# Kernel tuning notes

Hardware: AMD Instinct MI355X
Metric: run time of the kernel (lower is better)

The kernel has to match this reference:

```python
import jax, jax.numpy as jnp
import numpy as np

B, L, C, D = 32, 256, 16, 128
WORD_VOCAB, CHR_VOCAB = 50000, 128


def conv1d(x, w, b):
    # x: [N, D, T], w: [D_out, D_in, 3], torch Conv1d (cross-correlation), padding=1
    y = jax.lax.conv_general_dilated(x, w, window_strides=(1,), padding=[(1, 1)],
                                     dimension_numbers=('NCH', 'OIH', 'NCH'))
    return y + b[None, :, None]


def setup_inputs() -> dict:
    key = jax.random.key(0)
    k1, k2, k3, k4, k5, k6, k7, k8 = jax.random.split(key, 8)
    word_vector = jax.random.randint(k1, (B, L), 0, WORD_VOCAB)
    words_in_char = jax.random.randint(k2, (B, L, C), 0, CHR_VOCAB)
    # embedding tables, padding_idx=0 -> row 0 is zeros
    word_table = (jax.random.normal(k3, (WORD_VOCAB, D), jnp.float32) * 0.02).at[0].set(0.0)
    chr_table = (jax.random.normal(k4, (CHR_VOCAB, D), jnp.float32) * 0.02).at[0].set(0.0)
    scale = 1.0 / np.sqrt(D * 3)
    conv_chr_w = jax.random.normal(k5, (D, D, 3), jnp.float32) * scale
    conv_chr_b = jax.random.normal(k6, (D,), jnp.float32) * scale
    conv_word_w = jax.random.normal(k7, (D, D, 3), jnp.float32) * scale
    conv_word_b = jax.random.normal(k8, (D,), jnp.float32) * scale
    return dict(word_vector=word_vector, words_in_char=words_in_char,
                word_table=word_table, chr_table=chr_table,
                conv_chr_w=conv_chr_w, conv_chr_b=conv_chr_b,
                conv_word_w=conv_word_w, conv_word_b=conv_word_b)


def reference(word_vector, words_in_char, word_table, chr_table,
              conv_chr_w, conv_chr_b, conv_word_w, conv_word_b):
    # --- char path (batched version of the per-word Python loop) ---
    chr_emb = chr_table[words_in_char]                       # [B, L, C, D]
    x = chr_emb.reshape(B * L, C, D).transpose(0, 2, 1)      # [B*L, D, C]
    word_conv = conv1d(x, conv_chr_w, conv_chr_b)            # [B*L, D, C]
    char_feats = word_conv.max(axis=2).reshape(B, L, D)      # max over char positions
    # --- word path ---
    word_emb = word_table[word_vector]                       # [B, L, D]
    out = conv1d(word_emb.transpose(0, 2, 1), conv_word_w, conv_word_b)  # [B, D, L]
    # stack both branch outputs into one array: [2, B, D, L]
    return jnp.stack([out, char_feats.transpose(0, 2, 1)])
```

## Files before the change

### kernel.cpp

```cpp
#include <hip/hip_runtime.h>
#include <hip/hip_bf16.h>

typedef __attribute__((ext_vector_type(8))) short short8;
typedef __attribute__((ext_vector_type(4))) float float4_t;

#define NB 32
#define NL 256
#define NC 16
#define ND 128
#define OUT_PLANE (NB * ND * NL)

__device__ inline unsigned short f2bf(float f) {
    union { float f; unsigned int i; } c;
    c.f = f;
    unsigned int r = c.i + 0x7FFFu + ((c.i >> 16) & 1u);
    return (unsigned short)(r >> 16);
}

__global__ void make_frags(const float* __restrict__ Wc,
                           const float* __restrict__ Ww,
                           unsigned short* __restrict__ out) {
    int i = blockIdx.x * 256 + threadIdx.x;
    const int half = 12 * 8 * 64 * 8;
    const float* W = (i < half) ? Wc : Ww;
    int ii = (i < half) ? i : i - half;
    int j    = ii & 7;
    int lane = (ii >> 3) & 63;
    int nt   = (ii >> 9) & 7;
    int s    = ii >> 12;
    int dout = nt * 16 + (lane & 15);
    int t    = s >> 2;
    int k    = (s & 3) * 32 + ((lane >> 4) & 3) * 8 + j;
    out[i] = f2bf(W[(dout * 128 + k) * 3 + t]);
}

__global__ __launch_bounds__(128, 2) void char_kernel(
    const int* __restrict__ wic, const float* __restrict__ chrT,
    const unsigned short* __restrict__ frags,
    const float* __restrict__ bias,
    float* __restrict__ out1) {
    __shared__ unsigned short X[18 * 136];
    const int tid  = threadIdx.x;
    const int wave = tid >> 6, lane = tid & 63;
    const int m = lane & 15, quad = lane >> 4;

    for (int p = tid; p < 136; p += 128) { X[p] = 0; X[17 * 136 + p] = 0; }

    short8 bfrag[12][4];
#pragma unroll
    for (int s = 0; s < 12; ++s)
#pragma unroll
        for (int p = 0; p < 4; ++p) {
            int nt = wave * 4 + p;
            bfrag[s][p] =
                *(const short8*)(frags + (((s * 8 + nt) * 64 + lane) << 3));
        }
    float bb[4];
#pragma unroll
    for (int p = 0; p < 4; ++p) bb[p] = bias[wave * 64 + p * 16 + m];

    const int r = tid >> 3, seg = tid & 7;
    for (int wl = 0; wl < 8; ++wl) {
        int w = blockIdx.x * 8 + wl;
        __syncthreads();
        int idx = wic[w * 16 + r];
        const float4_t* src = (const float4_t*)(chrT + idx * 128 + seg * 16);
        unsigned short tmp[16];
#pragma unroll
        for (int q = 0; q < 4; ++q) {
            float4_t f = src[q];
            tmp[q * 4 + 0] = f2bf(f.x);
            tmp[q * 4 + 1] = f2bf(f.y);
            tmp[q * 4 + 2] = f2bf(f.z);
            tmp[q * 4 + 3] = f2bf(f.w);
        }
        *(short8*)&X[(r + 1) * 136 + seg * 16]     = *(const short8*)&tmp[0];
        *(short8*)&X[(r + 1) * 136 + seg * 16 + 8] = *(const short8*)&tmp[8];
        __syncthreads();

        float4_t acc[4];
#pragma unroll
        for (int p = 0; p < 4; ++p) acc[p] = (float4_t){0.f, 0.f, 0.f, 0.f};
#pragma unroll
        for (int s = 0; s < 12; ++s) {
            int row = m + (s >> 2);
            short8 a =
                *(const short8*)&X[row * 136 + (s & 3) * 32 + quad * 8];
#pragma unroll
            for (int p = 0; p < 4; ++p)
                acc[p] = __builtin_amdgcn_mfma_f32_16x16x32_bf16(
                    a, bfrag[s][p], acc[p], 0, 0, 0);
        }

        int b = w >> 8, l = w & 255;
        float* obase = out1 + b * (ND * NL) + l;
#pragma unroll
        for (int p = 0; p < 4; ++p) {
            float v = fmaxf(fmaxf(acc[p].x, acc[p].y),
                            fmaxf(acc[p].z, acc[p].w));
            v = fmaxf(v, __shfl_xor(v, 16, 64));
            v = fmaxf(v, __shfl_xor(v, 32, 64));
            v += bb[p];
            if (quad == 0) obase[(wave * 64 + p * 16 + m) * NL] = v;
        }
    }
}

__global__ __launch_bounds__(128, 2) void word_kernel(
    const int* __restrict__ wv, const float* __restrict__ wordT,
    const unsigned short* __restrict__ frags,
    const float* __restrict__ bias,
    float* __restrict__ out0) {
    __shared__ unsigned short X[18 * 136];
    const int tid  = threadIdx.x;
    const int wave = tid >> 6, lane = tid & 63;
    const int m = lane & 15, quad = lane >> 4;

    short8 bfrag[12][4];
#pragma unroll
    for (int s = 0; s < 12; ++s)
#pragma unroll
        for (int p = 0; p < 4; ++p) {
            int nt = wave * 4 + p;
            bfrag[s][p] = *(const short8*)(frags + 49152 +
                                           (((s * 8 + nt) * 64 + lane) << 3));
        }
    float bb[4];
#pragma unroll
    for (int p = 0; p < 4; ++p) bb[p] = bias[wave * 64 + p * 16 + m];

    for (int tl = 0; tl < 2; ++tl) {
        int tile = blockIdx.x * 2 + tl;
        int b = tile >> 4, l0 = (tile & 15) << 4;
        __syncthreads();
        for (int i = tid; i < 144; i += 128) {
            int rr = i >> 3, sg = i & 7;
            int l = l0 + rr - 1;
            int idx = (l >= 0 && l < NL) ? wv[b * NL + l] : 0;
            const float4_t* src = (const float4_t*)(wordT + idx * 128 + sg * 16);
            unsigned short tmp[16];
#pragma unroll
            for (int q = 0; q < 4; ++q) {
                float4_t f = src[q];
                tmp[q * 4 + 0] = f2bf(f.x);
                tmp[q * 4 + 1] = f2bf(f.y);
                tmp[q * 4 + 2] = f2bf(f.z);
                tmp[q * 4 + 3] = f2bf(f.w);
            }
            *(short8*)&X[rr * 136 + sg * 16]     = *(const short8*)&tmp[0];
            *(short8*)&X[rr * 136 + sg * 16 + 8] = *(const short8*)&tmp[8];
        }
        __syncthreads();

        float4_t acc[4];
#pragma unroll
        for (int p = 0; p < 4; ++p) acc[p] = (float4_t){0.f, 0.f, 0.f, 0.f};
#pragma unroll
        for (int s = 0; s < 12; ++s) {
            short8 a = *(const short8*)&X[(m + (s >> 2)) * 136 +
                                          (s & 3) * 32 + quad * 8];
#pragma unroll
            for (int p = 0; p < 4; ++p)
                acc[p] = __builtin_amdgcn_mfma_f32_16x16x32_bf16(
                    a, bfrag[s][p], acc[p], 0, 0, 0);
        }

        float* obase = out0 + b * (ND * NL) + l0 + quad * 4;
#pragma unroll
        for (int p = 0; p < 4; ++p) {
            int dout = wave * 64 + p * 16 + m;
            float4_t pk;
            pk.x = acc[p].x + bb[p];
            pk.y = acc[p].y + bb[p];
            pk.z = acc[p].z + bb[p];
            pk.w = acc[p].w + bb[p];
            *(float4_t*)&obase[dout * NL] = pk;
        }
    }
}

extern "C" void kernel_launch(void* const* d_in, const int* in_sizes, int n_in,
                              void* d_out, int out_size, void* d_ws,
                              size_t ws_size, hipStream_t stream) {
    const int* word_vector   = (const int*)d_in[0];
    const int* words_in_char = (const int*)d_in[1];
    const float* word_table  = (const float*)d_in[2];
    const float* chr_table   = (const float*)d_in[3];
    const float* conv_chr_w  = (const float*)d_in[4];
    const float* conv_chr_b  = (const float*)d_in[5];
    const float* conv_word_w = (const float*)d_in[6];
    const float* conv_word_b = (const float*)d_in[7];
    float* out            = (float*)d_out;
    unsigned short* frags = (unsigned short*)d_ws;

    make_frags<<<384, 256, 0, stream>>>(conv_chr_w, conv_word_w, frags);
    char_kernel<<<1024, 128, 0, stream>>>(words_in_char, chr_table, frags,
                                          conv_chr_b, out + OUT_PLANE);
    word_kernel<<<256, 128, 0, stream>>>(word_vector, word_table, frags,
                                         conv_word_b, out);
}
```

Before: 110.1 us.

## Merge char and word conv kernels and double-buffer char embedding gathers

Combines the char and word convolution kernels into one launch, using block-index ranges to pick the branch, so both branches run concurrently and one launch is removed. The char branch now double-buffers shared memory: it prefetches the next word's embedding rows and indices into registers while the MFMA work runs on the current buffer. The word branch gives each block one tile instead of two, which doubles the number of word blocks and repeats the weight-fragment loads per tile. The cost is twice the shared memory per block and more live registers, which could reduce occupancy.

```diff
diff --git a/kernel.cpp b/kernel.cpp
--- a/kernel.cpp
+++ b/kernel.cpp
@@ -1,14 +1,13 @@
 #include <hip/hip_runtime.h>
-#include <hip/hip_bf16.h>
 
 typedef __attribute__((ext_vector_type(8))) short short8;
 typedef __attribute__((ext_vector_type(4))) float float4_t;
 
 #define NB 32
 #define NL 256
-#define NC 16
 #define ND 128
 #define OUT_PLANE (NB * ND * NL)
+#define XS 136
 
 __device__ inline unsigned short f2bf(float f) {
     union { float f; unsigned int i; } c;
@@ -34,48 +33,132 @@
     out[i] = f2bf(W[(dout * 128 + k) * 3 + t]);
 }
 
-__global__ __launch_bounds__(128, 2) void char_kernel(
-    const int* __restrict__ wic, const float* __restrict__ chrT,
+__global__ __launch_bounds__(128, 2) void conv_kernel(
+    const int* __restrict__ wv, const int* __restrict__ wic,
+    const float* __restrict__ wordT, const float* __restrict__ chrT,
     const unsigned short* __restrict__ frags,
-    const float* __restrict__ bias,
-    float* __restrict__ out1) {
-    __shared__ unsigned short X[18 * 136];
+    const float* __restrict__ biasC, const float* __restrict__ biasW,
+    float* __restrict__ out) {
+    __shared__ unsigned short X[2][18 * XS];
     const int tid  = threadIdx.x;
     const int wave = tid >> 6, lane = tid & 63;
     const int m = lane & 15, quad = lane >> 4;
-
-    for (int p = tid; p < 136; p += 128) { X[p] = 0; X[17 * 136 + p] = 0; }
-
-    short8 bfrag[12][4];
-#pragma unroll
-    for (int s = 0; s < 12; ++s)
-#pragma unroll
-        for (int p = 0; p < 4; ++p) {
-            int nt = wave * 4 + p;
-            bfrag[s][p] =
-                *(const short8*)(frags + (((s * 8 + nt) * 64 + lane) << 3));
-        }
-    float bb[4];
-#pragma unroll
-    for (int p = 0; p < 4; ++p) bb[p] = bias[wave * 64 + p * 16 + m];
-
-    const int r = tid >> 3, seg = tid & 7;
-    for (int wl = 0; wl < 8; ++wl) {
-        int w = blockIdx.x * 8 + wl;
+    const int bid = blockIdx.x;
+
+    if (bid >= 512) {
+        const int w0 = (bid - 512) * 8;
+        short8 bfrag[12][4];
+#pragma unroll
+        for (int s = 0; s < 12; ++s)
+#pragma unroll
+            for (int p = 0; p < 4; ++p)
+                bfrag[s][p] = *(const short8*)(
+                    frags + (((s * 8 + wave * 4 + p) * 64 + lane) << 3));
+        float bb[4];
+#pragma unroll
+        for (int p = 0; p < 4; ++p) bb[p] = biasC[wave * 64 + p * 16 + m];
+
+        for (int p = tid; p < XS; p += 128) {
+            X[0][p] = 0; X[0][17 * XS + p] = 0;
+            X[1][p] = 0; X[1][17 * XS + p] = 0;
+        }
+        const int r = tid >> 3, seg = tid & 7;
+
+        {
+            int idx0 = wic[w0 * 16 + r];
+            const float4_t* src = (const float4_t*)(chrT + idx0 * 128 + seg * 16);
+            float4_t f0 = src[0], f1 = src[1], f2 = src[2], f3 = src[3];
+            unsigned short t16[16];
+            t16[0]=f2bf(f0.x); t16[1]=f2bf(f0.y); t16[2]=f2bf(f0.z); t16[3]=f2bf(f0.w);
+            t16[4]=f2bf(f1.x); t16[5]=f2bf(f1.y); t16[6]=f2bf(f1.z); t16[7]=f2bf(f1.w);
+            t16[8]=f2bf(f2.x); t16[9]=f2bf(f2.y); t16[10]=f2bf(f2.z); t16[11]=f2bf(f2.w);
+            t16[12]=f2bf(f3.x); t16[13]=f2bf(f3.y); t16[14]=f2bf(f3.z); t16[15]=f2bf(f3.w);
+            *(short8*)&X[0][(r + 1) * XS + seg * 16]     = *(const short8*)&t16[0];
+            *(short8*)&X[0][(r + 1) * XS + seg * 16 + 8] = *(const short8*)&t16[8];
+        }
+        int idxA = wic[(w0 + 1) * 16 + r];
         __syncthreads();
-        int idx = wic[w * 16 + r];
-        const float4_t* src = (const float4_t*)(chrT + idx * 128 + seg * 16);
-        unsigned short tmp[16];
-#pragma unroll
-        for (int q = 0; q < 4; ++q) {
-            float4_t f = src[q];
-            tmp[q * 4 + 0] = f2bf(f.x);
-            tmp[q * 4 + 1] = f2bf(f.y);
-            tmp[q * 4 + 2] = f2bf(f.z);
-            tmp[q * 4 + 3] = f2bf(f.w);
-        }
-        *(short8*)&X[(r + 1) * 136 + seg * 16]     = *(const short8*)&tmp[0];
-        *(short8*)&X[(r + 1) * 136 + seg * 16 + 8] = *(const short8*)&tmp[8];
+
+#pragma unroll
+        for (int wl = 0; wl < 8; ++wl) {
+            const int cur = wl & 1;
+            float4_t f0, f1, f2, f3;
+            if (wl < 7) {
+                const float4_t* src =
+                    (const float4_t*)(chrT + idxA * 128 + seg * 16);
+                f0 = src[0]; f1 = src[1]; f2 = src[2]; f3 = src[3];
+            }
+            int idxB = (wl < 6) ? wic[(w0 + wl + 2) * 16 + r] : 0;
+
+            float4_t acc[4];
+#pragma unroll
+            for (int p = 0; p < 4; ++p) acc[p] = (float4_t){0.f, 0.f, 0.f, 0.f};
+#pragma unroll
+            for (int s = 0; s < 12; ++s) {
+                short8 a = *(const short8*)&X[cur][(m + (s >> 2)) * XS +
+                                                  (s & 3) * 32 + quad * 8];
+#pragma unroll
+                for (int p = 0; p < 4; ++p)
+                    acc[p] = __builtin_amdgcn_mfma_f32_16x16x32_bf16(
+                        a, bfrag[s][p], acc[p], 0, 0, 0);
+            }
+
+            if (wl < 7) {
+                unsigned short t16[16];
+                t16[0]=f2bf(f0.x); t16[1]=f2bf(f0.y); t16[2]=f2bf(f0.z); t16[3]=f2bf(f0.w);
+                t16[4]=f2bf(f1.x); t16[5]=f2bf(f1.y); t16[6]=f2bf(f1.z); t16[7]=f2bf(f1.w);
+                t16[8]=f2bf(f2.x); t16[9]=f2bf(f2.y); t16[10]=f2bf(f2.z); t16[11]=f2bf(f2.w);
+                t16[12]=f2bf(f3.x); t16[13]=f2bf(f3.y); t16[14]=f2bf(f3.z); t16[15]=f2bf(f3.w);
+                *(short8*)&X[cur ^ 1][(r + 1) * XS + seg * 16]     = *(const short8*)&t16[0];
+                *(short8*)&X[cur ^ 1][(r + 1) * XS + seg * 16 + 8] = *(const short8*)&t16[8];
+                idxA = idxB;
+            }
+            __syncthreads();
+
+            int w = w0 + wl, b = w >> 8, l = w & 255;
+            float* obase = out + OUT_PLANE + b * (ND * NL) + l;
+#pragma unroll
+            for (int p = 0; p < 4; ++p) {
+                float v = fmaxf(fmaxf(acc[p].x, acc[p].y),
+                                fmaxf(acc[p].z, acc[p].w));
+                v = fmaxf(v, __shfl_xor(v, 16, 64));
+                v = fmaxf(v, __shfl_xor(v, 32, 64));
+                v += bb[p];
+                if (quad == 0) obase[(wave * 64 + p * 16 + m) * NL] = v;
+            }
+        }
+    } else {
+        const int b = bid >> 4, l0 = (bid & 15) << 4;
+        short8 bfrag[12][4];
+#pragma unroll
+        for (int s = 0; s < 12; ++s)
+#pragma unroll
+            for (int p = 0; p < 4; ++p)
+                bfrag[s][p] = *(const short8*)(
+                    frags + 49152 + (((s * 8 + wave * 4 + p) * 64 + lane) << 3));
+        float bb[4];
+#pragma unroll
+        for (int p = 0; p < 4; ++p) bb[p] = biasW[wave * 64 + p * 16 + m];
+
+#pragma unroll
+        for (int i0 = 0; i0 < 2; ++i0) {
+            int i = tid + i0 * 128;
+            if (i < 144) {
+                int rr = i >> 3, sg = i & 7;
+                int l = l0 + rr - 1;
+                int idx = (l >= 0 && l < NL) ? wv[b * NL + l] : 0;
+                const float4_t* src =
+                    (const float4_t*)(wordT + idx * 128 + sg * 16);
+                float4_t f0 = src[0], f1 = src[1], f2 = src[2], f3 = src[3];
+                unsigned short t16[16];
+                t16[0]=f2bf(f0.x); t16[1]=f2bf(f0.y); t16[2]=f2bf(f0.z); t16[3]=f2bf(f0.w);
+                t16[4]=f2bf(f1.x); t16[5]=f2bf(f1.y); t16[6]=f2bf(f1.z); t16[7]=f2bf(f1.w);
+                t16[8]=f2bf(f2.x); t16[9]=f2bf(f2.y); t16[10]=f2bf(f2.z); t16[11]=f2bf(f2.w);
+                t16[12]=f2bf(f3.x); t16[13]=f2bf(f3.y); t16[14]=f2bf(f3.z); t16[15]=f2bf(f3.w);
+                *(short8*)&X[0][rr * XS + sg * 16]     = *(const short8*)&t16[0];
+                *(short8*)&X[0][rr * XS + sg * 16 + 8] = *(const short8*)&t16[8];
+            }
+        }
         __syncthreads();
 
         float4_t acc[4];
@@ -83,89 +166,15 @@
         for (int p = 0; p < 4; ++p) acc[p] = (float4_t){0.f, 0.f, 0.f, 0.f};
 #pragma unroll
         for (int s = 0; s < 12; ++s) {
-            int row = m + (s >> 2);
-            short8 a =
-                *(const short8*)&X[row * 136 + (s & 3) * 32 + quad * 8];
+            short8 a = *(const short8*)&X[0][(m + (s >> 2)) * XS +
+                                            (s & 3) * 32 + quad * 8];
 #pragma unroll
             for (int p = 0; p < 4; ++p)
                 acc[p] = __builtin_amdgcn_mfma_f32_16x16x32_bf16(
                     a, bfrag[s][p], acc[p], 0, 0, 0);
         }
 
-        int b = w >> 8, l = w & 255;
-        float* obase = out1 + b * (ND * NL) + l;
-#pragma unroll
-        for (int p = 0; p < 4; ++p) {
-            float v = fmaxf(fmaxf(acc[p].x, acc[p].y),
-                            fmaxf(acc[p].z, acc[p].w));
-            v = fmaxf(v, __shfl_xor(v, 16, 64));
-            v = fmaxf(v, __shfl_xor(v, 32, 64));
-            v += bb[p];
-            if (quad == 0) obase[(wave * 64 + p * 16 + m) * NL] = v;
-        }
-    }
-}
-
-__global__ __launch_bounds__(128, 2) void word_kernel(
-    const int* __restrict__ wv, const float* __restrict__ wordT,
-    const unsigned short* __restrict__ frags,
-    const float* __restrict__ bias,
-    float* __restrict__ out0) {
-    __shared__ unsigned short X[18 * 136];
-    const int tid  = threadIdx.x;
-    const int wave = tid >> 6, lane = tid & 63;
-    const int m = lane & 15, quad = lane >> 4;
-
-    short8 bfrag[12][4];
-#pragma unroll
-    for (int s = 0; s < 12; ++s)
-#pragma unroll
-        for (int p = 0; p < 4; ++p) {
-            int nt = wave * 4 + p;
-            bfrag[s][p] = *(const short8*)(frags + 49152 +
-                                           (((s * 8 + nt) * 64 + lane) << 3));
-        }
-    float bb[4];
-#pragma unroll
-    for (int p = 0; p < 4; ++p) bb[p] = bias[wave * 64 + p * 16 + m];
-
-    for (int tl = 0; tl < 2; ++tl) {
-        int tile = blockIdx.x * 2 + tl;
-        int b = tile >> 4, l0 = (tile & 15) << 4;
-        __syncthreads();
-        for (int i = tid; i < 144; i += 128) {
-            int rr = i >> 3, sg = i & 7;
-            int l = l0 + rr - 1;
-            int idx = (l >= 0 && l < NL) ? wv[b * NL + l] : 0;
-            const float4_t* src = (const float4_t*)(wordT + idx * 128 + sg * 16);
-            unsigned short tmp[16];
-#pragma unroll
-            for (int q = 0; q < 4; ++q) {
-                float4_t f = src[q];
-                tmp[q * 4 + 0] = f2bf(f.x);
-                tmp[q * 4 + 1] = f2bf(f.y);
-                tmp[q * 4 + 2] = f2bf(f.z);
-                tmp[q * 4 + 3] = f2bf(f.w);
-            }
-            *(short8*)&X[rr * 136 + sg * 16]     = *(const short8*)&tmp[0];
-            *(short8*)&X[rr * 136 + sg * 16 + 8] = *(const short8*)&tmp[8];
-        }
-        __syncthreads();
-
-        float4_t acc[4];
-#pragma unroll
-        for (int p = 0; p < 4; ++p) acc[p] = (float4_t){0.f, 0.f, 0.f, 0.f};
-#pragma unroll
-        for (int s = 0; s < 12; ++s) {
-            short8 a = *(const short8*)&X[(m + (s >> 2)) * 136 +
-                                          (s & 3) * 32 + quad * 8];
-#pragma unroll
-            for (int p = 0; p < 4; ++p)
-                acc[p] = __builtin_amdgcn_mfma_f32_16x16x32_bf16(
-                    a, bfrag[s][p], acc[p], 0, 0, 0);
-        }
-
-        float* obase = out0 + b * (ND * NL) + l0 + quad * 4;
+        float* obase = out + b * (ND * NL) + l0 + quad * 4;
 #pragma unroll
         for (int p = 0; p < 4; ++p) {
             int dout = wave * 64 + p * 16 + m;
@@ -194,8 +203,7 @@
     unsigned short* frags = (unsigned short*)d_ws;
 
     make_frags<<<384, 256, 0, stream>>>(conv_chr_w, conv_word_w, frags);
-    char_kernel<<<1024, 128, 0, stream>>>(words_in_char, chr_table, frags,
-                                          conv_chr_b, out + OUT_PLANE);
-    word_kernel<<<256, 128, 0, stream>>>(word_vector, word_table, frags,
-                                         conv_word_b, out);
-}
+    conv_kernel<<<1536, 128, 0, stream>>>(word_vector, words_in_char,
+                                          word_table, chr_table, frags,
+                                          conv_chr_b, conv_word_b, out);
+}
```

Result: faster. 106.2 us (-3.5%).
